# Optimization experiments

Hardware: AMD Instinct MI355X
Metric: run time of the kernel (lower is better)

The kernel has to match this reference:

```python
import jax, jax.numpy as jnp
import numpy as np

N_NODES = 50000
N_EDGES = 800000
D_NODE = 128
D_EDGE = 16
HID = 128
BN_EPS = 1e-5


def gcn_conv(h, src, dst, W, b):
    # PyG GCNConv: h' = D^-1/2 (A + I) D^-1/2 (h W) + b, deg includes self-loop
    h = h @ W
    deg = jax.ops.segment_sum(jnp.ones((src.shape[0],), h.dtype), dst,
                              num_segments=N_NODES) + 1.0
    dinv = deg ** -0.5
    norm = dinv[src] * dinv[dst]                      # [E]
    agg = jax.ops.segment_sum(h[src] * norm[:, None], dst,
                              num_segments=N_NODES)   # scatter to dst
    agg = agg + h * (dinv * dinv)[:, None]            # self-loop term
    return agg + b


def setup_inputs() -> dict:
    key = jax.random.key(0)
    ks = jax.random.split(key, 12)
    s = lambda fan_in: 1.0 / np.sqrt(fan_in)
    return {
        "x": jax.random.normal(ks[0], (N_NODES, D_NODE), jnp.float32),
        "edge_index": jax.random.randint(ks[1], (2, N_EDGES), 0, N_NODES, jnp.int32),
        "edge_attr": jax.random.normal(ks[2], (N_EDGES, D_EDGE), jnp.float32),
        "W1": jax.random.normal(ks[3], (D_NODE, HID), jnp.float32) * s(D_NODE),
        "b1": jnp.zeros((HID,), jnp.float32),
        "gamma": jnp.ones((HID,), jnp.float32),
        "beta": jnp.zeros((HID,), jnp.float32),
        "W2": jax.random.normal(ks[4], (HID, HID), jnp.float32) * s(HID),
        "b2": jnp.zeros((HID,), jnp.float32),
        "Wm1": jax.random.normal(ks[5], (2 * HID + D_EDGE, HID), jnp.float32) * s(2 * HID + D_EDGE),
        "bm1": jnp.zeros((HID,), jnp.float32),
        "Wm2": jax.random.normal(ks[6], (HID, 1), jnp.float32) * s(HID),
        "bm2": jnp.zeros((1,), jnp.float32),
    }


def reference(x, edge_index, edge_attr, W1, b1, gamma, beta, W2, b2, Wm1, bm1, Wm2, bm2):
    src, dst = edge_index[0], edge_index[1]
    z = gcn_conv(x, src, dst, W1, b1)
    # BatchNorm1d over nodes (training-mode batch stats, biased var)
    mean = jnp.mean(z, axis=0)
    var = jnp.mean(jnp.square(z - mean), axis=0)
    z = (z - mean) * jax.lax.rsqrt(var + BN_EPS) * gamma + beta
    z = jax.nn.relu(z)
    z = gcn_conv(z, src, dst, W2, b2)
    # edge head: gather endpoints, concat with edge_attr, 2-layer MLP (dropout = eval identity)
    edge_input = jnp.concatenate([z[src], z[dst], edge_attr], axis=1)  # [E, 2H+De]
    h = jax.nn.relu(edge_input @ Wm1 + bm1)
    return (h @ Wm2 + bm2).squeeze(-1)  # [E]
```

## Files before the change

kernel.cpp:

```cpp
#include <hip/hip_runtime.h>
#include <hip/hip_bf16.h>

#define NN 50000
#define NE 800000
#define H 128
#define DE 16
#define BN_EPS 1e-5f
#define NB_SCAN 196

typedef float v2f __attribute__((ext_vector_type(2)));
typedef float v4f __attribute__((ext_vector_type(4)));
typedef short bfrag __attribute__((ext_vector_type(8)));

__device__ __forceinline__ unsigned int packbf2(float a, float b) {
    __hip_bfloat162 h = __float22bfloat162_rn(make_float2(a, b));
    return *(unsigned int*)&h;
}
__device__ __forceinline__ v2f unpackbf2(unsigned int u) {
    v2f r;
    r.x = __uint_as_float(u << 16);
    r.y = __uint_as_float(u & 0xffff0000u);
    return r;
}
__device__ __forceinline__ bfrag cvt8(float4 a0, float4 a1) {
    union { uint4 u; bfrag f; } x;
    x.u.x = packbf2(a0.x, a0.y);
    x.u.y = packbf2(a0.z, a0.w);
    x.u.z = packbf2(a1.x, a1.y);
    x.u.w = packbf2(a1.z, a1.w);
    return x.f;
}
__device__ __forceinline__ bfrag cvt8v(v4f a0, v4f a1) {
    union { uint4 u; bfrag f; } x;
    x.u.x = packbf2(a0.x, a0.y);
    x.u.y = packbf2(a0.z, a0.w);
    x.u.z = packbf2(a1.x, a1.y);
    x.u.w = packbf2(a1.z, a1.w);
    return x.f;
}
#define COMP(u4, j) ((j) == 0 ? (u4).x : (j) == 1 ? (u4).y : (j) == 2 ? (u4).z : (u4).w)

__device__ __forceinline__ float dpp_rowred16(float s) {
    s += __int_as_float(__builtin_amdgcn_update_dpp(0, __float_as_int(s), 0x121, 0xf, 0xf, false));
    s += __int_as_float(__builtin_amdgcn_update_dpp(0, __float_as_int(s), 0x122, 0xf, 0xf, false));
    s += __int_as_float(__builtin_amdgcn_update_dpp(0, __float_as_int(s), 0x124, 0xf, 0xf, false));
    s += __int_as_float(__builtin_amdgcn_update_dpp(0, __float_as_int(s), 0x128, 0xf, 0xf, false));
    return s;
}

__global__ void hist_k(const int* __restrict__ dst, int* __restrict__ counts) {
    int e = blockIdx.x * 256 + threadIdx.x;
    if (e < NE) atomicAdd(&counts[dst[e]], 1);
}

__global__ void scan1_k(const int* __restrict__ counts, int* __restrict__ bsum) {
    __shared__ int sh[256];
    int i = blockIdx.x * 256 + threadIdx.x;
    int v = (i < NN) ? counts[i] : 0;
    sh[threadIdx.x] = v;
    __syncthreads();
    for (int off = 128; off; off >>= 1) {
        if (threadIdx.x < off) sh[threadIdx.x] += sh[threadIdx.x + off];
        __syncthreads();
    }
    if (!threadIdx.x) bsum[blockIdx.x] = sh[0];
}

__global__ void scan2_k(int* __restrict__ bsum) {
    __shared__ int sh[256];
    int t = threadIdx.x;
    int v = (t < NB_SCAN) ? bsum[t] : 0;
    sh[t] = v;
    __syncthreads();
    for (int off = 1; off < 256; off <<= 1) {
        int x = (t >= off) ? sh[t - off] : 0;
        __syncthreads();
        sh[t] += x;
        __syncthreads();
    }
    if (t < NB_SCAN) bsum[t] = sh[t] - v;
}

__global__ void scan3_k(const int* __restrict__ counts, const int* __restrict__ bsum,
                        int* __restrict__ offsets, int* __restrict__ cursor,
                        float* __restrict__ dinv) {
    __shared__ int sh[256];
    int i = blockIdx.x * 256 + threadIdx.x;
    int v = (i < NN) ? counts[i] : 0;
    sh[threadIdx.x] = v;
    __syncthreads();
    for (int off = 1; off < 256; off <<= 1) {
        int x = (threadIdx.x >= off) ? sh[threadIdx.x - off] : 0;
        __syncthreads();
        sh[threadIdx.x] += x;
        __syncthreads();
    }
    if (i < NN) {
        int excl = sh[threadIdx.x] - v + bsum[blockIdx.x];
        offsets[i] = excl;
        cursor[i] = excl;
        dinv[i] = rsqrtf((float)v + 1.0f);
    }
}

__global__ void fill_k(const int* __restrict__ src, const int* __restrict__ dst,
                       int* __restrict__ cursor, int* __restrict__ srcs) {
    int e = blockIdx.x * 256 + threadIdx.x;
    if (e < NE) {
        int d = dst[e];
        int pos = atomicAdd(&cursor[d], 1);
        srcs[pos] = src[e];
    }
}

__global__ void cvtAll_k(const float* __restrict__ W1, const float* __restrict__ W2,
                         const float* __restrict__ Ws, const float* __restrict__ Wd,
                         const float* __restrict__ We,
                         short* __restrict__ d1, short* __restrict__ d2,
                         short* __restrict__ ds_, short* __restrict__ dd,
                         unsigned int* __restrict__ WePk) {
    int b = blockIdx.x;
    if (b < 256) {
        int mat = b >> 6;
        const float* s = mat == 0 ? W1 : mat == 1 ? W2 : mat == 2 ? Ws : Wd;
        short* d = mat == 0 ? d1 : mat == 1 ? d2 : mat == 2 ? ds_ : dd;
        int idx = (b & 63) * 256 + threadIdx.x;
        int n = idx & 127, k = idx >> 7;
        float v = s[k * 128 + n];
        d[n * 128 + k] = (short)(packbf2(v, v) & 0xffff);
    } else {
        int idx = (b - 256) * 256 + threadIdx.x;
        int c = idx >> 8;
        int lane = (idx >> 2) & 63;
        int j2 = (idx & 3) * 2;
        int q = lane >> 4, i = lane & 15;
        int k0 = q * 8 + j2, k1 = k0 + 1;
        int feat = i * 8 + c;
        float v0 = (k0 < 16) ? We[k0 * 128 + feat] : 0.f;
        float v1 = (k1 < 16) ? We[k1 * 128 + feat] : 0.f;
        WePk[idx] = packbf2(v0, v1);
    }
}

__global__ __launch_bounds__(256) void gemm_mfma(const float* __restrict__ A,
                                                 const unsigned int* __restrict__ Ab,
                                                 const short* __restrict__ Bt,
                                                 unsigned int* __restrict__ Cb,
                                                 const float* __restrict__ rowScale,
                                                 const float* __restrict__ tA,
                                                 const float* __restrict__ tC,
                                                 int M) {
    int lane = threadIdx.x & 63;
    int w = threadIdx.x >> 6;
    int i = lane & 15;
    int q = lane >> 4;
    int r0 = blockIdx.x * 64 + w * 16;
    int arow = min(r0 + i, M - 1);

    v4f acc[8];
#pragma unroll
    for (int c = 0; c < 8; c++) acc[c] = (v4f)0.f;

#pragma unroll
    for (int kc = 0; kc < 128; kc += 32) {
        int kb = kc + q * 8;
        bfrag af;
        if (Ab) {
            uint4 u = *(const uint4*)&Ab[(size_t)arow * 64 + (kb >> 1)];
            v2f z0 = unpackbf2(u.x), z1 = unpackbf2(u.y);
            v2f z2 = unpackbf2(u.z), z3 = unpackbf2(u.w);
            v2f t0 = *(const v2f*)&tA[kb],     c0 = *(const v2f*)&tC[kb];
            v2f t1 = *(const v2f*)&tA[kb + 2], c1 = *(const v2f*)&tC[kb + 2];
            v2f t2 = *(const v2f*)&tA[kb + 4], c2 = *(const v2f*)&tC[kb + 4];
            v2f t3 = *(const v2f*)&tA[kb + 6], c3 = *(const v2f*)&tC[kb + 6];
            z0 = z0 * t0 + c0; z1 = z1 * t1 + c1;
            z2 = z2 * t2 + c2; z3 = z3 * t3 + c3;
            union { uint4 u; bfrag f; } x;
            x.u.x = packbf2(fmaxf(z0.x, 0.f), fmaxf(z0.y, 0.f));
            x.u.y = packbf2(fmaxf(z1.x, 0.f), fmaxf(z1.y, 0.f));
            x.u.z = packbf2(fmaxf(z2.x, 0.f), fmaxf(z2.y, 0.f));
            x.u.w = packbf2(fmaxf(z3.x, 0.f), fmaxf(z3.y, 0.f));
            af = x.f;
        } else {
            const float* Arow = A + (size_t)arow * 128;
            float4 a0 = *(const float4*)&Arow[kb];
            float4 a1 = *(const float4*)&Arow[kb + 4];
            af = cvt8(a0, a1);
        }
#pragma unroll
        for (int c = 0; c < 8; c++) {
            bfrag bf = *(const bfrag*)&Bt[(size_t)(c * 16 + i) * 128 + kb];
            acc[c] = __builtin_amdgcn_mfma_f32_16x16x32_bf16(af, bf, acc[c], 0, 0, 0);
        }
    }

    int orow0 = r0 + q * 4;
    v4f ds = (v4f)1.f;
    if (rowScale) ds = *(const v4f*)&rowScale[min(orow0, M - 4)];
#pragma unroll
    for (int c = 0; c < 8; c++) {
        int col = c * 16 + i;
#pragma unroll
        for (int r = 0; r < 4; r++) {
            float v = acc[c][r] * ds[r];
            float vp = __shfl_xor(v, 1, 64);
            if (!(i & 1) && orow0 + r < M)
                Cb[(size_t)(orow0 + r) * 64 + (col >> 1)] = packbf2(v, vp);
        }
    }
}

__global__ __launch_bounds__(256) void gemm_pq(const unsigned int* __restrict__ zbA,
                                               const short* __restrict__ Bs_,
                                               const short* __restrict__ Bd_,
                                               const float* __restrict__ bm1,
                                               unsigned int* __restrict__ Pb,
                                               unsigned int* __restrict__ Qb,
                                               int M) {
    int lane = threadIdx.x & 63;
    int w = threadIdx.x >> 6;
    int i = lane & 15;
    int q = lane >> 4;
    int r0 = blockIdx.x * 64 + w * 16;
    int arow = min(r0 + i, M - 1);

    v4f accP[8], accQ[8];
#pragma unroll
    for (int c = 0; c < 8; c++) { accP[c] = (v4f)0.f; accQ[c] = (v4f)0.f; }

#pragma unroll
    for (int kc = 0; kc < 128; kc += 32) {
        int kb = kc + q * 8;
        bfrag af = *(const bfrag*)&zbA[(size_t)arow * 64 + (kb >> 1)];
#pragma unroll
        for (int c = 0; c < 8; c++) {
            bfrag bs = *(const bfrag*)&Bs_[(size_t)(c * 16 + i) * 128 + kb];
            bfrag bd = *(const bfrag*)&Bd_[(size_t)(c * 16 + i) * 128 + kb];
            accP[c] = __builtin_amdgcn_mfma_f32_16x16x32_bf16(af, bs, accP[c], 0, 0, 0);
            accQ[c] = __builtin_amdgcn_mfma_f32_16x16x32_bf16(af, bd, accQ[c], 0, 0, 0);
        }
    }

    int orow0 = r0 + q * 4;
    float bm1c[8];
#pragma unroll
    for (int c = 0; c < 8; c++) bm1c[c] = bm1[c * 16 + i];
#pragma unroll
    for (int c = 0; c < 8; c++) {
        int col = c * 16 + i;
#pragma unroll
        for (int r = 0; r < 4; r++) {
            float vP = accP[c][r];
            float vPp = __shfl_xor(vP, 1, 64);
            float vQ = accQ[c][r] + bm1c[c];
            float vQp = __shfl_xor(vQ, 1, 64);
            if (!(i & 1) && orow0 + r < M) {
                Pb[(size_t)(orow0 + r) * 64 + (col >> 1)] = packbf2(vP, vPp);
                Qb[(size_t)(orow0 + r) * 64 + (col >> 1)] = packbf2(vQ, vQp);
            }
        }
    }
}

__global__ __launch_bounds__(256) void aggregate_k(const unsigned int* __restrict__ hsb,
                                                   const int* __restrict__ offsets,
                                                   const int* __restrict__ counts,
                                                   const int* __restrict__ srcs,
                                                   const float* __restrict__ dinv,
                                                   const float* __restrict__ bias,
                                                   unsigned int* __restrict__ zbout) {
    int lane = threadIdx.x & 63;
    int i = lane & 15;
    int q = lane >> 4;
    int n = __builtin_amdgcn_readfirstlane(blockIdx.x * 4 + (threadIdx.x >> 6));
    if (n >= NN) return;
    int beg = offsets[n];
    int cnt = counts[n];
    v2f A0 = {0.f, 0.f}, A1 = {0.f, 0.f}, A2 = {0.f, 0.f}, A3 = {0.f, 0.f};
    v2f B0 = {0.f, 0.f}, B1 = {0.f, 0.f}, B2 = {0.f, 0.f}, B3 = {0.f, 0.f};
    for (int c = 0; c < cnt; c += 64) {
        int vsrc = srcs[beg + c + lane];
        int m = min(64, cnt - c);
        int ngrp = m >> 2;
        int g = 0;
        for (; g + 4 <= ngrp; g += 4) {
            int s0 = __shfl(vsrc, g * 4 + q, 64);
            int s1 = __shfl(vsrc, g * 4 + 4 + q, 64);
            int s2 = __shfl(vsrc, g * 4 + 8 + q, 64);
            int s3 = __shfl(vsrc, g * 4 + 12 + q, 64);
            uint4 u0 = *(const uint4*)&hsb[(size_t)s0 * 64 + i * 4];
            uint4 u1 = *(const uint4*)&hsb[(size_t)s1 * 64 + i * 4];
            uint4 u2 = *(const uint4*)&hsb[(size_t)s2 * 64 + i * 4];
            uint4 u3 = *(const uint4*)&hsb[(size_t)s3 * 64 + i * 4];
            A0 += unpackbf2(u0.x); A1 += unpackbf2(u0.y); A2 += unpackbf2(u0.z); A3 += unpackbf2(u0.w);
            B0 += unpackbf2(u1.x); B1 += unpackbf2(u1.y); B2 += unpackbf2(u1.z); B3 += unpackbf2(u1.w);
            A0 += unpackbf2(u2.x); A1 += unpackbf2(u2.y); A2 += unpackbf2(u2.z); A3 += unpackbf2(u2.w);
            B0 += unpackbf2(u3.x); B1 += unpackbf2(u3.y); B2 += unpackbf2(u3.z); B3 += unpackbf2(u3.w);
        }
        for (; g < ngrp; g++) {
            int s0 = __shfl(vsrc, g * 4 + q, 64);
            uint4 u0 = *(const uint4*)&hsb[(size_t)s0 * 64 + i * 4];
            A0 += unpackbf2(u0.x); A1 += unpackbf2(u0.y); A2 += unpackbf2(u0.z); A3 += unpackbf2(u0.w);
        }
        int rem = m & 3;
        if (rem) {
            int s0 = __shfl(vsrc, (m & ~3) + q, 64);
            if (q < rem) {
                uint4 u0 = *(const uint4*)&hsb[(size_t)s0 * 64 + i * 4];
                B0 += unpackbf2(u0.x); B1 += unpackbf2(u0.y); B2 += unpackbf2(u0.z); B3 += unpackbf2(u0.w);
            }
        }
    }
    A0 += B0; A1 += B1; A2 += B2; A3 += B3;
    A0.x += __shfl_xor(A0.x, 32, 64); A0.y += __shfl_xor(A0.y, 32, 64);
    A1.x += __shfl_xor(A1.x, 32, 64); A1.y += __shfl_xor(A1.y, 32, 64);
    A2.x += __shfl_xor(A2.x, 32, 64); A2.y += __shfl_xor(A2.y, 32, 64);
    A3.x += __shfl_xor(A3.x, 32, 64); A3.y += __shfl_xor(A3.y, 32, 64);
    bool hi = (lane & 32) != 0;
    v2f U0, U1;
    U0.x = hi ? A2.x : A0.x; U0.y = hi ? A2.y : A0.y;
    U1.x = hi ? A3.x : A1.x; U1.y = hi ? A3.y : A1.y;
    U0.x += __shfl_xor(U0.x, 16, 64); U0.y += __shfl_xor(U0.y, 16, 64);
    U1.x += __shfl_xor(U1.x, 16, 64); U1.y += __shfl_xor(U1.y, 16, 64);
    bool lo = (lane & 16) != 0;
    v2f res;
    res.x = lo ? U1.x : U0.x;
    res.y = lo ? U1.y : U0.y;
    int ui = i * 4 + q;
    v2f self = unpackbf2(hsb[(size_t)n * 64 + ui]);
    float di = dinv[n];
    float2 b = *(const float2*)&bias[ui * 2];
    float rx = (res.x + self.x) * di + b.x;
    float ry = (res.y + self.y) * di + b.y;
    zbout[(size_t)n * 64 + ui] = packbf2(rx, ry);
}

__global__ __launch_bounds__(256) void bnstats_b_k(const unsigned int* __restrict__ zb,
                                                   float* __restrict__ sums,
                                                   float* __restrict__ sumsq) {
    __shared__ v2f ls[4][64], lq[4][64];
    int lane = threadIdx.x & 63;
    int sub = threadIdx.x >> 6;
    v2f s = {0.f, 0.f}, q = {0.f, 0.f};
    for (int r = blockIdx.x * 4 + sub; r < NN; r += gridDim.x * 4) {
        v2f v = unpackbf2(zb[(size_t)r * 64 + lane]);
        s += v;
        q += v * v;
    }
    if (sub) { ls[sub][lane] = s; lq[sub][lane] = q; }
    __syncthreads();
    if (!sub) {
        s += ls[1][lane] + ls[2][lane] + ls[3][lane];
        q += lq[1][lane] + lq[2][lane] + lq[3][lane];
        atomicAdd(&sums[lane * 2], s.x);
        atomicAdd(&sums[lane * 2 + 1], s.y);
        atomicAdd(&sumsq[lane * 2], q.x);
        atomicAdd(&sumsq[lane * 2 + 1], q.y);
    }
}

__global__ void bnfinal_k(const float* __restrict__ sums, const float* __restrict__ sumsq,
                          const float* __restrict__ gamma, const float* __restrict__ beta,
                          float* __restrict__ bnA, float* __restrict__ bnC) {
    int f = threadIdx.x;
    if (f < 128) {
        float mean = sums[f] * (1.0f / NN);
        float var = sumsq[f] * (1.0f / NN) - mean * mean;
        float a = gamma[f] * rsqrtf(var + BN_EPS);
        bnA[f] = a;
        bnC[f] = beta[f] - mean * a;
    }
}

__global__ __launch_bounds__(256) void edgehead_k(const unsigned int* __restrict__ Pb,
                                                  const unsigned int* __restrict__ Qb,
                                                  const float* __restrict__ ea,
                                                  const int* __restrict__ srcI,
                                                  const int* __restrict__ dstI,
                                                  const unsigned int* __restrict__ WePk,
                                                  const float* __restrict__ Wm2,
                                                  const float* __restrict__ bm2,
                                                  float* __restrict__ out) {
    int lane = threadIdx.x & 63;
    int wid = threadIdx.x >> 6;
    int base = (blockIdx.x * 4 + wid) * 64;
    int i = lane & 15;
    int q = lane >> 4;

    bfrag wef[8];
#pragma unroll
    for (int c = 0; c < 8; c++)
        wef[c] = *(const bfrag*)&WePk[(c * 64 + lane) * 4];
    float4 wv0 = *(const float4*)&Wm2[i * 8];
    float4 wv1 = *(const float4*)&Wm2[i * 8 + 4];
    v2f wv2[4];
    wv2[0].x = wv0.x; wv2[0].y = wv0.y;
    wv2[1].x = wv0.z; wv2[1].y = wv0.w;
    wv2[2].x = wv1.x; wv2[2].y = wv1.y;
    wv2[3].x = wv1.z; wv2[3].y = wv1.w;
    float bm2v = bm2[0];

    int sv = srcI[base + lane];
    int dv = dstI[base + lane];

#pragma unroll
    for (int t = 0; t < 4; t++) {
        int tb = t * 16;
        bfrag af;
#pragma unroll
        for (int z = 0; z < 8; z++) af[z] = 0;
        if (q < 2) {
            const float* erow = &ea[(size_t)(base + tb + i) * 16 + q * 8];
            v4f e0 = __builtin_nontemporal_load((const v4f*)erow);
            v4f e1 = __builtin_nontemporal_load((const v4f*)(erow + 4));
            af = cvt8v(e0, e1);
        }
        uint4 Pu[4], Qu[4];
#pragma unroll
        for (int r = 0; r < 4; r++) {
            int sr = __shfl(sv, tb + q * 4 + r, 64);
            int dr = __shfl(dv, tb + q * 4 + r, 64);
            Pu[r] = *(const uint4*)&Pb[(size_t)sr * 64 + i * 4];
            Qu[r] = *(const uint4*)&Qb[(size_t)dr * 64 + i * 4];
        }
        v4f acc[8];
#pragma unroll
        for (int c = 0; c < 8; c++) acc[c] = (v4f)0.f;
#pragma unroll
        for (int c = 0; c < 8; c++)
            acc[c] = __builtin_amdgcn_mfma_f32_16x16x32_bf16(af, wef[c], acc[c], 0, 0, 0);
#pragma unroll
        for (int r = 0; r < 4; r++) {
            v2f sa = {0.f, 0.f};
#pragma unroll
            for (int j = 0; j < 4; j++) {
                v2f pq = unpackbf2(COMP(Pu[r], j)) + unpackbf2(COMP(Qu[r], j));
                v2f tt;
                tt.x = acc[2 * j][r] + pq.x;
                tt.y = acc[2 * j + 1][r] + pq.y;
                tt.x = fmaxf(tt.x, 0.f);
                tt.y = fmaxf(tt.y, 0.f);
                sa += tt * wv2[j];
            }
            float s = dpp_rowred16(sa.x + sa.y);
            if (i == 0) __builtin_nontemporal_store(s + bm2v, &out[base + tb + q * 4 + r]);
        }
    }
}

extern "C" void kernel_launch(void* const* d_in, const int* in_sizes, int n_in,
                              void* d_out, int out_size, void* d_ws, size_t ws_size,
                              hipStream_t stream) {
    const float* x     = (const float*)d_in[0];
    const int*   ei    = (const int*)d_in[1];
    const float* ea    = (const float*)d_in[2];
    const float* W1    = (const float*)d_in[3];
    const float* b1    = (const float*)d_in[4];
    const float* gamma = (const float*)d_in[5];
    const float* beta  = (const float*)d_in[6];
    const float* W2    = (const float*)d_in[7];
    const float* b2    = (const float*)d_in[8];
    const float* Wm1   = (const float*)d_in[9];
    const float* bm1   = (const float*)d_in[10];
    const float* Wm2   = (const float*)d_in[11];
    const float* bm2   = (const float*)d_in[12];
    float* out = (float*)d_out;

    const int* srcI = ei;
    const int* dstI = ei + NE;

    char* w = (char*)d_ws;
    auto alloc = [&](size_t bytes) {
        char* p = w;
        w += (bytes + 255) & ~(size_t)255;
        return p;
    };
    float* dinv    = (float*)alloc(NN * 4);
    int*   counts  = (int*)alloc(NN * 4);
    int*   offsets = (int*)alloc(NN * 4);
    int*   cursor  = (int*)alloc(NN * 4);
    int*   bsum    = (int*)alloc(256 * 4);
    int*   srcs    = (int*)alloc((size_t)(NE + 64) * 4);
    float* sums    = (float*)alloc(128 * 4);
    float* sumsq   = (float*)alloc(128 * 4);
    float* bnA     = (float*)alloc(128 * 4);
    float* bnC     = (float*)alloc(128 * 4);
    short* bt1     = (short*)alloc(128 * 128 * 2);
    short* bt2     = (short*)alloc(128 * 128 * 2);
    short* bts     = (short*)alloc(128 * 128 * 2);
    short* btd     = (short*)alloc(128 * 128 * 2);
    unsigned int* WePk = (unsigned int*)alloc(2048 * 4);
    unsigned int* hsb  = (unsigned int*)alloc((size_t)NN * 64 * 4);
    unsigned int* zb1  = (unsigned int*)alloc((size_t)NN * 64 * 4);
    unsigned int* Qb   = (unsigned int*)alloc((size_t)NN * 64 * 4);
    unsigned int* zb2  = zb1;

    hipMemsetAsync(counts, 0, NN * 4, stream);
    hipMemsetAsync(sums, 0, 128 * 4, stream);
    hipMemsetAsync(sumsq, 0, 128 * 4, stream);

    hist_k<<<(NE + 255) / 256, 256, 0, stream>>>(dstI, counts);
    scan1_k<<<NB_SCAN, 256, 0, stream>>>(counts, bsum);
    scan2_k<<<1, 256, 0, stream>>>(bsum);
    scan3_k<<<NB_SCAN, 256, 0, stream>>>(counts, bsum, offsets, cursor, dinv);
    fill_k<<<(NE + 255) / 256, 256, 0, stream>>>(srcI, dstI, cursor, srcs);
    cvtAll_k<<<264, 256, 0, stream>>>(W1, W2, Wm1, Wm1 + 128 * 128, Wm1 + 256 * 128,
                                      bt1, bt2, bts, btd, WePk);

    const int GB = (NN + 63) / 64;
    const int AGG = (NN + 3) / 4;

    gemm_mfma<<<GB, 256, 0, stream>>>(x, nullptr, bt1, hsb, dinv, nullptr, nullptr, NN);
    aggregate_k<<<AGG, 256, 0, stream>>>(hsb, offsets, counts, srcs, dinv, b1, zb1);

    bnstats_b_k<<<256, 256, 0, stream>>>(zb1, sums, sumsq);
    bnfinal_k<<<1, 128, 0, stream>>>(sums, sumsq, gamma, beta, bnA, bnC);

    gemm_mfma<<<GB, 256, 0, stream>>>(nullptr, zb1, bt2, hsb, dinv, bnA, bnC, NN);
    aggregate_k<<<AGG, 256, 0, stream>>>(hsb, offsets, counts, srcs, dinv, b2, zb2);

    gemm_pq<<<GB, 256, 0, stream>>>(zb2, bts, btd, bm1, hsb, Qb, NN);

    edgehead_k<<<NE / 256, 256, 0, stream>>>(hsb, Qb, ea, srcI, dstI, WePk,
                                             Wm2, bm2, out);
}
```

Measured before the change: 449.2 us.

## Fuse small setup kernels to cut launch count and memsets

Merges the histogram with the weight conversion, folds scan2 into scan3, runs the CSR fill alongside the first GEMM in a single grid, and computes the BatchNorm affine coefficients inside the second GEMM's prologue. The three memsets become one by placing counts and the BN sums contiguously. The goal is to remove several tiny kernel launches and the gaps between them. In exchange, every scan23 block redundantly scans the block sums, and every gemm_bn block recomputes the BN coefficients.

```diff
diff --git a/kernel.cpp b/kernel.cpp
--- a/kernel.cpp
+++ b/kernel.cpp
@@ -7,6 +7,7 @@
 #define DE 16
 #define BN_EPS 1e-5f
 #define NB_SCAN 196
+#define NB_E 3125
 
 typedef float v2f __attribute__((ext_vector_type(2)));
 typedef float v4f __attribute__((ext_vector_type(4)));
@@ -48,78 +49,23 @@
     return s;
 }
 
-__global__ void hist_k(const int* __restrict__ dst, int* __restrict__ counts) {
-    int e = blockIdx.x * 256 + threadIdx.x;
-    if (e < NE) atomicAdd(&counts[dst[e]], 1);
-}
-
-__global__ void scan1_k(const int* __restrict__ counts, int* __restrict__ bsum) {
-    __shared__ int sh[256];
-    int i = blockIdx.x * 256 + threadIdx.x;
-    int v = (i < NN) ? counts[i] : 0;
-    sh[threadIdx.x] = v;
-    __syncthreads();
-    for (int off = 128; off; off >>= 1) {
-        if (threadIdx.x < off) sh[threadIdx.x] += sh[threadIdx.x + off];
-        __syncthreads();
-    }
-    if (!threadIdx.x) bsum[blockIdx.x] = sh[0];
-}
-
-__global__ void scan2_k(int* __restrict__ bsum) {
-    __shared__ int sh[256];
-    int t = threadIdx.x;
-    int v = (t < NB_SCAN) ? bsum[t] : 0;
-    sh[t] = v;
-    __syncthreads();
-    for (int off = 1; off < 256; off <<= 1) {
-        int x = (t >= off) ? sh[t - off] : 0;
-        __syncthreads();
-        sh[t] += x;
-        __syncthreads();
-    }
-    if (t < NB_SCAN) bsum[t] = sh[t] - v;
-}
-
-__global__ void scan3_k(const int* __restrict__ counts, const int* __restrict__ bsum,
-                        int* __restrict__ offsets, int* __restrict__ cursor,
-                        float* __restrict__ dinv) {
-    __shared__ int sh[256];
-    int i = blockIdx.x * 256 + threadIdx.x;
-    int v = (i < NN) ? counts[i] : 0;
-    sh[threadIdx.x] = v;
-    __syncthreads();
-    for (int off = 1; off < 256; off <<= 1) {
-        int x = (threadIdx.x >= off) ? sh[threadIdx.x - off] : 0;
-        __syncthreads();
-        sh[threadIdx.x] += x;
-        __syncthreads();
-    }
-    if (i < NN) {
-        int excl = sh[threadIdx.x] - v + bsum[blockIdx.x];
-        offsets[i] = excl;
-        cursor[i] = excl;
-        dinv[i] = rsqrtf((float)v + 1.0f);
-    }
-}
-
-__global__ void fill_k(const int* __restrict__ src, const int* __restrict__ dst,
-                       int* __restrict__ cursor, int* __restrict__ srcs) {
-    int e = blockIdx.x * 256 + threadIdx.x;
-    if (e < NE) {
-        int d = dst[e];
-        int pos = atomicAdd(&cursor[d], 1);
-        srcs[pos] = src[e];
-    }
-}
-
-__global__ void cvtAll_k(const float* __restrict__ W1, const float* __restrict__ W2,
-                         const float* __restrict__ Ws, const float* __restrict__ Wd,
-                         const float* __restrict__ We,
-                         short* __restrict__ d1, short* __restrict__ d2,
-                         short* __restrict__ ds_, short* __restrict__ dd,
-                         unsigned int* __restrict__ WePk) {
+__global__ __launch_bounds__(256) void histcvt_k(const int* __restrict__ dst,
+                                                 int* __restrict__ counts,
+                                                 const float* __restrict__ W1,
+                                                 const float* __restrict__ W2,
+                                                 const float* __restrict__ Ws,
+                                                 const float* __restrict__ Wd,
+                                                 const float* __restrict__ We,
+                                                 short* __restrict__ d1, short* __restrict__ d2,
+                                                 short* __restrict__ ds_, short* __restrict__ dd,
+                                                 unsigned int* __restrict__ WePk) {
     int b = blockIdx.x;
+    if (b < NB_E) {
+        int e = b * 256 + threadIdx.x;
+        atomicAdd(&counts[dst[e]], 1);
+        return;
+    }
+    b -= NB_E;
     if (b < 256) {
         int mat = b >> 6;
         const float* s = mat == 0 ? W1 : mat == 1 ? W2 : mat == 2 ? Ws : Wd;
@@ -142,20 +88,134 @@
     }
 }
 
-__global__ __launch_bounds__(256) void gemm_mfma(const float* __restrict__ A,
-                                                 const unsigned int* __restrict__ Ab,
+__global__ void scan1_k(const int* __restrict__ counts, int* __restrict__ bsum) {
+    __shared__ int sh[256];
+    int i = blockIdx.x * 256 + threadIdx.x;
+    int v = (i < NN) ? counts[i] : 0;
+    sh[threadIdx.x] = v;
+    __syncthreads();
+    for (int off = 128; off; off >>= 1) {
+        if (threadIdx.x < off) sh[threadIdx.x] += sh[threadIdx.x + off];
+        __syncthreads();
+    }
+    if (!threadIdx.x) bsum[blockIdx.x] = sh[0];
+}
+
+__global__ void scan23_k(const int* __restrict__ counts, const int* __restrict__ bsum,
+                         int* __restrict__ offsets, int* __restrict__ cursor,
+                         float* __restrict__ dinv) {
+    __shared__ int bs[256];
+    __shared__ int sh[256];
+    int t = threadIdx.x;
+    int bv = (t < NB_SCAN) ? bsum[t] : 0;
+    bs[t] = bv;
+    __syncthreads();
+    for (int off = 1; off < 256; off <<= 1) {
+        int x = (t >= off) ? bs[t - off] : 0;
+        __syncthreads();
+        bs[t] += x;
+        __syncthreads();
+    }
+    int bexcl = (blockIdx.x > 0) ? bs[blockIdx.x - 1] : 0;
+    int i = blockIdx.x * 256 + t;
+    int v = (i < NN) ? counts[i] : 0;
+    sh[t] = v;
+    __syncthreads();
+    for (int off = 1; off < 256; off <<= 1) {
+        int x = (t >= off) ? sh[t - off] : 0;
+        __syncthreads();
+        sh[t] += x;
+        __syncthreads();
+    }
+    if (i < NN) {
+        int excl = sh[t] - v + bexcl;
+        offsets[i] = excl;
+        cursor[i] = excl;
+        dinv[i] = rsqrtf((float)v + 1.0f);
+    }
+}
+
+__global__ __launch_bounds__(256) void fillgemm_k(const int* __restrict__ src,
+                                                  const int* __restrict__ dst,
+                                                  int* __restrict__ cursor,
+                                                  int* __restrict__ srcs,
+                                                  const float* __restrict__ A,
+                                                  const short* __restrict__ Bt,
+                                                  unsigned int* __restrict__ Cb,
+                                                  const float* __restrict__ rowScale) {
+    if (blockIdx.x < NB_E) {
+        int e = blockIdx.x * 256 + threadIdx.x;
+        int d = dst[e];
+        int pos = atomicAdd(&cursor[d], 1);
+        srcs[pos] = src[e];
+        return;
+    }
+    int bid = blockIdx.x - NB_E;
+    int lane = threadIdx.x & 63;
+    int w = threadIdx.x >> 6;
+    int i = lane & 15;
+    int q = lane >> 4;
+    int r0 = bid * 64 + w * 16;
+    int arow = min(r0 + i, NN - 1);
+    const float* Arow = A + (size_t)arow * 128;
+
+    v4f acc[8];
+#pragma unroll
+    for (int c = 0; c < 8; c++) acc[c] = (v4f)0.f;
+
+#pragma unroll
+    for (int kc = 0; kc < 128; kc += 32) {
+        int kb = kc + q * 8;
+        float4 a0 = *(const float4*)&Arow[kb];
+        float4 a1 = *(const float4*)&Arow[kb + 4];
+        bfrag af = cvt8(a0, a1);
+#pragma unroll
+        for (int c = 0; c < 8; c++) {
+            bfrag bf = *(const bfrag*)&Bt[(size_t)(c * 16 + i) * 128 + kb];
+            acc[c] = __builtin_amdgcn_mfma_f32_16x16x32_bf16(af, bf, acc[c], 0, 0, 0);
+        }
+    }
+
+    int orow0 = r0 + q * 4;
+    v4f ds = *(const v4f*)&rowScale[min(orow0, NN - 4)];
+#pragma unroll
+    for (int c = 0; c < 8; c++) {
+        int col = c * 16 + i;
+#pragma unroll
+        for (int r = 0; r < 4; r++) {
+            float v = acc[c][r] * ds[r];
+            float vp = __shfl_xor(v, 1, 64);
+            if (!(i & 1) && orow0 + r < NN)
+                Cb[(size_t)(orow0 + r) * 64 + (col >> 1)] = packbf2(v, vp);
+        }
+    }
+}
+
+__global__ __launch_bounds__(256) void gemm_bn_k(const unsigned int* __restrict__ Ab,
                                                  const short* __restrict__ Bt,
                                                  unsigned int* __restrict__ Cb,
                                                  const float* __restrict__ rowScale,
-                                                 const float* __restrict__ tA,
-                                                 const float* __restrict__ tC,
-                                                 int M) {
+                                                 const float* __restrict__ sums,
+                                                 const float* __restrict__ sumsq,
+                                                 const float* __restrict__ gamma,
+                                                 const float* __restrict__ beta) {
+    __shared__ __align__(16) float tAs[128], tCs[128];
+    if (threadIdx.x < 128) {
+        int f = threadIdx.x;
+        float mean = sums[f] * (1.0f / NN);
+        float var = sumsq[f] * (1.0f / NN) - mean * mean;
+        float a = gamma[f] * rsqrtf(var + BN_EPS);
+        tAs[f] = a;
+        tCs[f] = beta[f] - mean * a;
+    }
+    __syncthreads();
+
     int lane = threadIdx.x & 63;
     int w = threadIdx.x >> 6;
     int i = lane & 15;
     int q = lane >> 4;
     int r0 = blockIdx.x * 64 + w * 16;
-    int arow = min(r0 + i, M - 1);
+    int arow = min(r0 + i, NN - 1);
 
     v4f acc[8];
 #pragma unroll
@@ -164,29 +224,21 @@
 #pragma unroll
     for (int kc = 0; kc < 128; kc += 32) {
         int kb = kc + q * 8;
-        bfrag af;
-        if (Ab) {
-            uint4 u = *(const uint4*)&Ab[(size_t)arow * 64 + (kb >> 1)];
-            v2f z0 = unpackbf2(u.x), z1 = unpackbf2(u.y);
-            v2f z2 = unpackbf2(u.z), z3 = unpackbf2(u.w);
-            v2f t0 = *(const v2f*)&tA[kb],     c0 = *(const v2f*)&tC[kb];
-            v2f t1 = *(const v2f*)&tA[kb + 2], c1 = *(const v2f*)&tC[kb + 2];
-            v2f t2 = *(const v2f*)&tA[kb + 4], c2 = *(const v2f*)&tC[kb + 4];
-            v2f t3 = *(const v2f*)&tA[kb + 6], c3 = *(const v2f*)&tC[kb + 6];
-            z0 = z0 * t0 + c0; z1 = z1 * t1 + c1;
-            z2 = z2 * t2 + c2; z3 = z3 * t3 + c3;
-            union { uint4 u; bfrag f; } x;
-            x.u.x = packbf2(fmaxf(z0.x, 0.f), fmaxf(z0.y, 0.f));
-            x.u.y = packbf2(fmaxf(z1.x, 0.f), fmaxf(z1.y, 0.f));
-            x.u.z = packbf2(fmaxf(z2.x, 0.f), fmaxf(z2.y, 0.f));
-            x.u.w = packbf2(fmaxf(z3.x, 0.f), fmaxf(z3.y, 0.f));
-            af = x.f;
-        } else {
-            const float* Arow = A + (size_t)arow * 128;
-            float4 a0 = *(const float4*)&Arow[kb];
-            float4 a1 = *(const float4*)&Arow[kb + 4];
-            af = cvt8(a0, a1);
-        }
+        uint4 u = *(const uint4*)&Ab[(size_t)arow * 64 + (kb >> 1)];
+        v2f z0 = unpackbf2(u.x), z1 = unpackbf2(u.y);
+        v2f z2 = unpackbf2(u.z), z3 = unpackbf2(u.w);
+        v2f t0 = *(const v2f*)&tAs[kb],     c0 = *(const v2f*)&tCs[kb];
+        v2f t1 = *(const v2f*)&tAs[kb + 2], c1 = *(const v2f*)&tCs[kb + 2];
+        v2f t2 = *(const v2f*)&tAs[kb + 4], c2 = *(const v2f*)&tCs[kb + 4];
+        v2f t3 = *(const v2f*)&tAs[kb + 6], c3 = *(const v2f*)&tCs[kb + 6];
+        z0 = z0 * t0 + c0; z1 = z1 * t1 + c1;
+        z2 = z2 * t2 + c2; z3 = z3 * t3 + c3;
+        union { uint4 u; bfrag f; } x;
+        x.u.x = packbf2(fmaxf(z0.x, 0.f), fmaxf(z0.y, 0.f));
+        x.u.y = packbf2(fmaxf(z1.x, 0.f), fmaxf(z1.y, 0.f));
+        x.u.z = packbf2(fmaxf(z2.x, 0.f), fmaxf(z2.y, 0.f));
+        x.u.w = packbf2(fmaxf(z3.x, 0.f), fmaxf(z3.y, 0.f));
+        bfrag af = x.f;
 #pragma unroll
         for (int c = 0; c < 8; c++) {
             bfrag bf = *(const bfrag*)&Bt[(size_t)(c * 16 + i) * 128 + kb];
@@ -195,8 +247,7 @@
     }
 
     int orow0 = r0 + q * 4;
-    v4f ds = (v4f)1.f;
-    if (rowScale) ds = *(const v4f*)&rowScale[min(orow0, M - 4)];
+    v4f ds = *(const v4f*)&rowScale[min(orow0, NN - 4)];
 #pragma unroll
     for (int c = 0; c < 8; c++) {
         int col = c * 16 + i;
@@ -204,7 +255,7 @@
         for (int r = 0; r < 4; r++) {
             float v = acc[c][r] * ds[r];
             float vp = __shfl_xor(v, 1, 64);
-            if (!(i & 1) && orow0 + r < M)
+            if (!(i & 1) && orow0 + r < NN)
                 Cb[(size_t)(orow0 + r) * 64 + (col >> 1)] = packbf2(v, vp);
         }
     }
@@ -359,19 +410,6 @@
     }
 }
 
-__global__ void bnfinal_k(const float* __restrict__ sums, const float* __restrict__ sumsq,
-                          const float* __restrict__ gamma, const float* __restrict__ beta,
-                          float* __restrict__ bnA, float* __restrict__ bnC) {
-    int f = threadIdx.x;
-    if (f < 128) {
-        float mean = sums[f] * (1.0f / NN);
-        float var = sumsq[f] * (1.0f / NN) - mean * mean;
-        float a = gamma[f] * rsqrtf(var + BN_EPS);
-        bnA[f] = a;
-        bnC[f] = beta[f] - mean * a;
-    }
-}
-
 __global__ __launch_bounds__(256) void edgehead_k(const unsigned int* __restrict__ Pb,
                                                   const unsigned int* __restrict__ Qb,
                                                   const float* __restrict__ ea,
@@ -475,16 +513,14 @@
         w += (bytes + 255) & ~(size_t)255;
         return p;
     };
+    int*   counts  = (int*)alloc((NN + 256) * 4);
+    float* sums    = (float*)(counts + NN);
+    float* sumsq   = sums + 128;
     float* dinv    = (float*)alloc(NN * 4);
-    int*   counts  = (int*)alloc(NN * 4);
     int*   offsets = (int*)alloc(NN * 4);
     int*   cursor  = (int*)alloc(NN * 4);
     int*   bsum    = (int*)alloc(256 * 4);
     int*   srcs    = (int*)alloc((size_t)(NE + 64) * 4);
-    float* sums    = (float*)alloc(128 * 4);
-    float* sumsq   = (float*)alloc(128 * 4);
-    float* bnA     = (float*)alloc(128 * 4);
-    float* bnC     = (float*)alloc(128 * 4);
     short* bt1     = (short*)alloc(128 * 128 * 2);
     short* bt2     = (short*)alloc(128 * 128 * 2);
     short* bts     = (short*)alloc(128 * 128 * 2);
@@ -495,32 +531,24 @@
     unsigned int* Qb   = (unsigned int*)alloc((size_t)NN * 64 * 4);
     unsigned int* zb2  = zb1;
 
-    hipMemsetAsync(counts, 0, NN * 4, stream);
-    hipMemsetAsync(sums, 0, 128 * 4, stream);
-    hipMemsetAsync(sumsq, 0, 128 * 4, stream);
-
-    hist_k<<<(NE + 255) / 256, 256, 0, stream>>>(dstI, counts);
+    hipMemsetAsync(counts, 0, (NN + 256) * 4, stream);
+
+    histcvt_k<<<NB_E + 264, 256, 0, stream>>>(dstI, counts, W1, W2, Wm1,
+                                              Wm1 + 128 * 128, Wm1 + 256 * 128,
+                                              bt1, bt2, bts, btd, WePk);
     scan1_k<<<NB_SCAN, 256, 0, stream>>>(counts, bsum);
-    scan2_k<<<1, 256, 0, stream>>>(bsum);
-    scan3_k<<<NB_SCAN, 256, 0, stream>>>(counts, bsum, offsets, cursor, dinv);
-    fill_k<<<(NE + 255) / 256, 256, 0, stream>>>(srcI, dstI, cursor, srcs);
-    cvtAll_k<<<264, 256, 0, stream>>>(W1, W2, Wm1, Wm1 + 128 * 128, Wm1 + 256 * 128,
-                                      bt1, bt2, bts, btd, WePk);
+    scan23_k<<<NB_SCAN, 256, 0, stream>>>(counts, bsum, offsets, cursor, dinv);
 
     const int GB = (NN + 63) / 64;
     const int AGG = (NN + 3) / 4;
 
-    gemm_mfma<<<GB, 256, 0, stream>>>(x, nullptr, bt1, hsb, dinv, nullptr, nullptr, NN);
+    fillgemm_k<<<NB_E + GB, 256, 0, stream>>>(srcI, dstI, cursor, srcs,
+                                              x, bt1, hsb, dinv);
     aggregate_k<<<AGG, 256, 0, stream>>>(hsb, offsets, counts, srcs, dinv, b1, zb1);
-
     bnstats_b_k<<<256, 256, 0, stream>>>(zb1, sums, sumsq);
-    bnfinal_k<<<1, 128, 0, stream>>>(sums, sumsq, gamma, beta, bnA, bnC);
-
-    gemm_mfma<<<GB, 256, 0, stream>>>(nullptr, zb1, bt2, hsb, dinv, bnA, bnC, NN);
+    gemm_bn_k<<<GB, 256, 0, stream>>>(zb1, bt2, hsb, dinv, sums, sumsq, gamma, beta);
     aggregate_k<<<AGG, 256, 0, stream>>>(hsb, offsets, counts, srcs, dinv, b2, zb2);
-
     gemm_pq<<<GB, 256, 0, stream>>>(zb2, bts, btd, bm1, hsb, Qb, NN);
-
-    edgehead_k<<<NE / 256, 256, 0, stream>>>(hsb, Qb, ea, srcI, dstI, WePk,
-                                             Wm2, bm2, out);
-}
+    edgehead_k<<<NB_E, 256, 0, stream>>>(hsb, Qb, ea, srcI, dstI, WePk,
+                                         Wm2, bm2, out);
+}
```

Result: no change. 447.9 us (-0.3%).
